# Performance work log

Measured on AMD Instinct MI355X. Metric: run time of the kernel, lower is better.

## Reference

```python
import jax, jax.numpy as jnp
import numpy as np

DIM = 1024
NUM_HEADS = 16
HEAD_DIM = DIM // NUM_HEADS
B, T = 2, 2048


def setup_inputs() -> dict:
    key = jax.random.key(0)
    ks = jax.random.split(key, 7)
    x = jax.random.normal(ks[0], (B, T, DIM), dtype=jnp.float32)
    # causal mask, broadcastable over batch and heads
    mask = jnp.tril(jnp.ones((T, T), dtype=bool))[None, None, :, :]
    # rope tables for half rotary angles, tiled to head_dim (cat of two halves)
    pos = jnp.arange(T, dtype=jnp.float32)[:, None]
    inv_freq = 1.0 / (10000.0 ** (jnp.arange(0, HEAD_DIM, 2, dtype=jnp.float32) / HEAD_DIM))
    ang = pos * inv_freq[None, :]                      # [T, hd/2]
    ang = jnp.concatenate([ang, ang], axis=-1)         # [T, hd]
    rope_sin = jnp.sin(ang)[None, None, :, :]
    rope_cos = jnp.cos(ang)[None, None, :, :]
    s = 0.02
    qkv_w = jax.random.normal(ks[1], (DIM, 3 * DIM), dtype=jnp.float32) * s
    qkv_b = jnp.zeros((3 * DIM,), dtype=jnp.float32)
    proj_w = jax.random.normal(ks[2], (DIM, DIM), dtype=jnp.float32) * s
    proj_b = jnp.zeros((DIM,), dtype=jnp.float32)
    return {"x": x, "mask": mask, "rope_sin": rope_sin, "rope_cos": rope_cos,
            "qkv_w": qkv_w, "qkv_b": qkv_b, "proj_w": proj_w, "proj_b": proj_b}


def _rotate_half(t):
    half = t.shape[-1] // 2
    return jnp.concatenate([-t[..., half:], t[..., :half]], axis=-1)


def _apply_rope(t, sin, cos):
    return t * cos + _rotate_half(t) * sin


def reference(x, mask, rope_sin, rope_cos, qkv_w, qkv_b, proj_w, proj_b):
    Bb, Tt, C = x.shape
    qkv = x @ qkv_w + qkv_b                            # [B, T, 3C]
    q, k, v = jnp.split(qkv, 3, axis=-1)
    def split_heads(t):                                # [B, T, C] -> [B, H, T, hd]
        return t.reshape(Bb, Tt, NUM_HEADS, HEAD_DIM).transpose(0, 2, 1, 3)
    q, k, v = split_heads(q), split_heads(k), split_heads(v)
    sin = rope_sin[:, :, :Tt, :]
    cos = rope_cos[:, :, :Tt, :]
    q = _apply_rope(q, sin, cos)
    k = _apply_rope(k, sin, cos)
    att = jnp.einsum("bhqd,bhkd->bhqk", q, k) / (HEAD_DIM ** 0.5)
    att = jnp.where(mask, att, -jnp.inf)
    att = jax.nn.softmax(att, axis=-1)
    y = jnp.einsum("bhqk,bhkd->bhqd", att, v)          # [B, H, T, hd]
    y = y.transpose(0, 2, 1, 3).reshape(Bb, Tt, C)
    return y @ proj_w + proj_b
```

## Files before the change

kernel.cpp:

```cpp
#include <hip/hip_runtime.h>

typedef unsigned short u16;
typedef u16 u16x8 __attribute__((ext_vector_type(8)));
typedef __bf16 bf16x8 __attribute__((ext_vector_type(8)));
typedef float f32x4 __attribute__((ext_vector_type(4)));

#define T_SEQ 2048
#define DIM 1024
#define NH 16
#define HD 64

#define MFMA(a, b, c) __builtin_amdgcn_mfma_f32_16x16x32_bf16(a, b, c, 0, 0, 0)

__device__ __forceinline__ u16 f2bf(float f) {
  return __builtin_bit_cast(u16, static_cast<__bf16>(f));
}

__device__ __forceinline__ bf16x8 ld8(const u16* p) {
  return __builtin_bit_cast(bf16x8, *(const u16x8*)p);
}

__device__ __forceinline__ void gload_lds16(const u16* g, u16* l) {
  __builtin_amdgcn_global_load_lds((const __attribute__((address_space(1))) void*)(g),
                                   (__attribute__((address_space(3))) void*)(l),
                                   16, 0, 0);
}

__global__ void k_prep(const float* __restrict__ X, u16* __restrict__ Y,
                       const float* __restrict__ Wq, u16* __restrict__ WqT,
                       const float* __restrict__ Wp, u16* __restrict__ WpT) {
  __shared__ float tile[32][33];
  int bid = blockIdx.x;
  if (bid < 4096) {
    int i = (bid * 256 + threadIdx.x) * 4;
    float4 f = *(const float4*)&X[i];
    ushort4 o = make_ushort4(f2bf(f.x), f2bf(f.y), f2bf(f.z), f2bf(f.w));
    *(ushort4*)&Y[i] = o;
    return;
  }
  const float* W; u16* WT; int K = 1024, N, bx, by;
  if (bid < 4096 + 3072) { int t = bid - 4096; W = Wq; WT = WqT; N = 3072; bx = t % 96; by = t / 96; }
  else                   { int t = bid - 7168; W = Wp; WT = WpT; N = 1024; bx = t % 32; by = t / 32; }
  int tx = threadIdx.x & 31, ty = threadIdx.x >> 5;
  int c0 = bx * 32, r0 = by * 32;
#pragma unroll
  for (int r = 0; r < 4; r++)
    tile[ty + r * 8][tx] = W[(r0 + ty + r * 8) * N + c0 + tx];
  __syncthreads();
#pragma unroll
  for (int r = 0; r < 4; r++)
    WT[(c0 + ty + r * 8) * K + r0 + tx] = f2bf(tile[tx][ty + r * 8]);
}


#define GEMM_STAGE3(buf, kk)                                                      \
  {                                                                               \
    _Pragma("unroll") for (int p = 0; p < 2; p++) {                               \
      int rr = w * 32 + p * 16;                                                   \
      gload_lds16(&Agp[(size_t)(rowBase + rr + srow) * Kd + (kk) + schunk],       \
                  &As[buf][rr * 32]);                                             \
      gload_lds16(&Bgp[(size_t)(colBase + rr + srow) * Kd + (kk) + schunk],       \
                  &Bs[buf][rr * 32]);                                             \
    }                                                                             \
  }

#define GEMM_COMPUTE3(buf)                                                        \
  {                                                                               \
    bf16x8 af[4], bfv[4];                                                         \
    _Pragma("unroll") for (int i = 0; i < 4; i++) {                               \
      af[i] = ld8(&As[buf][(wm * 64 + i * 16 + l15) * 32 + quad * 8]);            \
      bfv[i] = ld8(&Bs[buf][(wn * 64 + i * 16 + l15) * 32 + quad * 8]);           \
    }                                                                             \
    _Pragma("unroll") for (int i = 0; i < 4; i++)                                 \
        _Pragma("unroll") for (int j = 0; j < 4; j++)                             \
            acc[i][j] = MFMA(af[i], bfv[j], acc[i][j]);                           \
  }

#define GEMM_CORE3(Aptr, BTptr, bxv, byv)                                         \
  const int tid = threadIdx.x;                                                    \
  const int lane = tid & 63, w = tid >> 6;                                        \
  const int l15 = lane & 15, quad = lane >> 4;                                    \
  const int wm = w >> 1, wn = w & 1;                                              \
  const int rowBase = (byv) * 128;                                                \
  const int colBase = (bxv) * 128;                                                \
  const u16* Agp = (Aptr);                                                        \
  const u16* Bgp = (BTptr);                                                       \
  const int Kd = DIM;                                                             \
  f32x4 acc[4][4];                                                                \
  _Pragma("unroll") for (int i = 0; i < 4; i++)                                   \
      _Pragma("unroll") for (int j = 0; j < 4; j++)                               \
          acc[i][j] = (f32x4){0.f, 0.f, 0.f, 0.f};                                \
  const int srow = lane >> 2;                 \
  const int schunk = (lane & 3) * 8;    \
  GEMM_STAGE3(0, 0)                                                               \
  GEMM_STAGE3(1, 32)                                                              \
  _Pragma("unroll") for (int s = 0; s < 32; ++s) {                                \
    if (s < 31) { asm volatile("s_waitcnt vmcnt(4)" ::: "memory"); }              \
    else        { asm volatile("s_waitcnt vmcnt(0)" ::: "memory"); }              \
    __builtin_amdgcn_s_barrier();                                                 \
    if (s + 2 < 32) { GEMM_STAGE3((s + 2) % 3, (s + 2) * 32) }                    \
    GEMM_COMPUTE3(s % 3)                                                          \
  }                                                                               \
  __syncthreads();

#define EPLD 136

__global__ __launch_bounds__(256) void k_gemm_qkv(
    const u16* __restrict__ A, const u16* __restrict__ BT,
    const float* __restrict__ bias,
    const float* __restrict__ rsin, const float* __restrict__ rcos,
    u16* __restrict__ qb, u16* __restrict__ kb, u16* __restrict__ vtb) {
  __shared__ __align__(16) u16 LDSBUF[24576];
  u16 (*As)[128 * 32] = (u16(*)[128 * 32])(LDSBUF);
  u16 (*Bs)[128 * 32] = (u16(*)[128 * 32])(LDSBUF + 12288);
  const int n = blockIdx.x, xcd = n & 7, s = n >> 3;
  const int cg = xcd & 1, rg = xcd >> 1;
  const int bxv = cg * 12 + (s >> 3);
  const int byv = rg * 8 + (s & 7);
  GEMM_CORE3(A, BT, bxv, byv)

#pragma unroll
  for (int j = 0; j < 4; j++) {
    float bv = bias[colBase + wn * 64 + j * 16 + l15];
#pragma unroll
    for (int i = 0; i < 4; i++)
#pragma unroll
      for (int r = 0; r < 4; r++) acc[i][j][r] += bv;
  }

  const int colW = colBase + wn * 64;
  const int sec = colW >> 10;

  if (sec == 2) {
#pragma unroll
    for (int i = 0; i < 4; i++)
#pragma unroll
      for (int r = 0; r < 4; r++) {
        int tl = wm * 64 + i * 16 + quad * 4 + r;
#pragma unroll
        for (int j = 0; j < 4; j++) {
          int d2 = wn * 64 + j * 16 + l15;
          LDSBUF[d2 * EPLD + tl] = f2bf(acc[i][j][r]);
        }
      }
  } else {
#pragma unroll
    for (int i = 0; i < 4; i++)
#pragma unroll
      for (int r = 0; r < 4; r++) {
        int tl = wm * 64 + i * 16 + quad * 4 + r;
        int t = (rowBase + tl) & 2047;
#pragma unroll
        for (int j = 0; j < 4; j++) {
          int d = j * 16 + l15;
          float v = acc[i][j][r];
          float pr = acc[i][j ^ 2][r];
          float rot = (j < 2) ? -pr : pr;
          float rv = v * rcos[t * HD + d] + rot * rsin[t * HD + d];
          if (sec == 0) rv *= 0.18033688011112042f;
          LDSBUF[tl * EPLD + wn * 64 + d] = f2bf(rv);
        }
      }
  }
  __syncthreads();

  const int hb = (colBase & 1023) >> 6;
  const int b = rowBase >> 11, t0 = rowBase & 2047;
  if (sec == 2) {
#pragma unroll
    for (int p = 0; p < 8; p++) {
      int drow = (tid >> 4) + p * 16;
      int tc = (tid & 15) * 8;
      int hh = hb + (drow >> 6), d = drow & 63;
      u16x8 v = *(const u16x8*)&LDSBUF[drow * EPLD + tc];
      *(u16x8*)&vtb[((size_t)(b * NH + hh) * HD + d) * T_SEQ + t0 + tc] = v;
    }
  } else {
    u16* dst = (sec == 0) ? qb : kb;
#pragma unroll
    for (int p = 0; p < 8; p++) {
      int row = (tid >> 4) + p * 16;
      int dc = (tid & 15) * 8;
      int hh = hb + (dc >> 6), d = dc & 63;
      u16x8 v = *(const u16x8*)&LDSBUF[row * EPLD + dc];
      *(u16x8*)&dst[((size_t)(b * NH + hh) * T_SEQ + t0 + row) * HD + d] = v;
    }
  }
}

__global__ __launch_bounds__(256) void k_gemm_proj(
    const u16* __restrict__ A, const u16* __restrict__ BT,
    const float* __restrict__ bias, float* __restrict__ C) {
  __shared__ __align__(16) u16 AsP[3][4096];
  __shared__ __align__(16) u16 BsP[3][2048];
  const int n = blockIdx.x, xcd = n & 7, s = n >> 3;
  const int cg = xcd & 1, rg = xcd >> 1;
  const int bxv = cg * 8 + (s >> 3);
  const int byv = rg * 8 + (s & 7);
  const int tid = threadIdx.x;
  const int lane = tid & 63, w = tid >> 6;
  const int l15 = lane & 15, quad = lane >> 4;
  const int wm = w >> 1, wn = w & 1;
  const int rowBase = byv * 128;
  const int colBase = bxv * 64;
  const int srow = lane >> 2, schunk = (lane & 3) * 8;
  f32x4 acc[4][2];
#pragma unroll
  for (int i = 0; i < 4; i++)
#pragma unroll
    for (int j = 0; j < 2; j++) acc[i][j] = (f32x4){0.f, 0.f, 0.f, 0.f};

#define PROJ_STAGE(buf, kk)                                                       \
  {                                                                               \
    _Pragma("unroll") for (int p = 0; p < 2; p++) {                               \
      int rr = w * 32 + p * 16;                                                   \
      gload_lds16(&A[(size_t)(rowBase + rr + srow) * DIM + (kk) + schunk],        \
                  &AsP[buf][rr * 32]);                                            \
    }                                                                             \
    gload_lds16(&BT[(size_t)(colBase + w * 16 + srow) * DIM + (kk) + schunk],     \
                &BsP[buf][w * 16 * 32]);                                          \
  }
#define PROJ_COMPUTE(buf)                                                         \
  {                                                                               \
    bf16x8 af[4], bfv[2];                                                         \
    _Pragma("unroll") for (int i = 0; i < 4; i++)                                 \
        af[i] = ld8(&AsP[buf][(wm * 64 + i * 16 + l15) * 32 + quad * 8]);         \
    _Pragma("unroll") for (int j = 0; j < 2; j++)                                 \
        bfv[j] = ld8(&BsP[buf][(wn * 32 + j * 16 + l15) * 32 + quad * 8]);        \
    _Pragma("unroll") for (int i = 0; i < 4; i++)                                 \
        _Pragma("unroll") for (int j = 0; j < 2; j++)                             \
            acc[i][j] = MFMA(af[i], bfv[j], acc[i][j]);                           \
  }

  PROJ_STAGE(0, 0)
  PROJ_STAGE(1, 32)
#pragma unroll
  for (int s2 = 0; s2 < 32; ++s2) {
    if (s2 < 31) { asm volatile("s_waitcnt vmcnt(3)" ::: "memory"); }
    else         { asm volatile("s_waitcnt vmcnt(0)" ::: "memory"); }
    __builtin_amdgcn_s_barrier();
    if (s2 + 2 < 32) { PROJ_STAGE((s2 + 2) % 3, (s2 + 2) * 32) }
    PROJ_COMPUTE(s2 % 3)
  }

#pragma unroll
  for (int i = 0; i < 4; i++)
#pragma unroll
    for (int r = 0; r < 4; r++) {
      int grow = rowBase + wm * 64 + i * 16 + quad * 4 + r;
#pragma unroll
      for (int j = 0; j < 2; j++) {
        int col = colBase + wn * 32 + j * 16 + l15;
        C[grow * DIM + col] = acc[i][j][r] + bias[col];
      }
    }
}

#define KLD 72
#define VLD 136

__global__ __launch_bounds__(256, 3) void k_attn(
    const u16* __restrict__ qb, const u16* __restrict__ kb,
    const u16* __restrict__ vtb, u16* __restrict__ yb) {
  __shared__ __align__(16) u16 Ks[128 * KLD];
  __shared__ __align__(16) u16 VTs[64 * VLD];
  __shared__ __align__(16) u16 Ps[64 * VLD];
  const int tid = threadIdx.x;
  const int lane = tid & 63, w = tid >> 6;
  const int l15 = lane & 15, quad = lane >> 4;
  const int bh = blockIdx.x;
  const int qt = 31 - blockIdx.y;

  const u16* qp = qb + (size_t)bh * T_SEQ * HD;
  const u16* kp = kb + (size_t)bh * T_SEQ * HD;
  const u16* vp = vtb + (size_t)bh * HD * T_SEQ;

  const int nch = (qt + 2) >> 1;
  const int qrow_base = qt * 64 + w * 16 + quad * 4;

  const int sr = tid >> 3, sc = (tid & 7) * 8;
  const int vr = tid >> 4, vc = (tid & 15) * 8;

  u16x8 kreg[4], vreg[4];
#define LOADKV(c)                                                              \
  {                                                                            \
    _Pragma("unroll") for (int p = 0; p < 4; p++)                              \
        kreg[p] = *(const u16x8*)&kp[((c) * 128 + sr + p * 32) * HD + sc];     \
    _Pragma("unroll") for (int p = 0; p < 4; p++)                              \
        vreg[p] = *(const u16x8*)&vp[(vr + p * 16) * T_SEQ + (c) * 128 + vc];  \
  }
#define WRITEK()                                                               \
  {                                                                            \
    _Pragma("unroll") for (int p = 0; p < 4; p++)                              \
        *(u16x8*)&Ks[(sr + p * 32) * KLD + sc] = kreg[p];                      \
  }
#define WRITEV()                                                               \
  {                                                                            \
    _Pragma("unroll") for (int p = 0; p < 4; p++)                              \
        *(u16x8*)&VTs[(vr + p * 16) * VLD + vc] = vreg[p];                     \
  }

  LOADKV(0)

  {
#pragma unroll
    for (int p = 0; p < 2; p++) {
      int r = sr + p * 32;
      *(u16x8*)&Ps[r * KLD + sc] = *(const u16x8*)&qp[(qt * 64 + r) * HD + sc];
    }
  }
  __syncthreads();
  bf16x8 qa0 = ld8(&Ps[(w * 16 + l15) * KLD + quad * 8]);
  bf16x8 qa1 = ld8(&Ps[(w * 16 + l15) * KLD + 32 + quad * 8]);
  WRITEK()
  WRITEV()
  __syncthreads();

  f32x4 o[4];
#pragma unroll
  for (int j = 0; j < 4; j++) o[j] = (f32x4){0.f, 0.f, 0.f, 0.f};
  float li[4] = {0.f, 0.f, 0.f, 0.f};

  u16* ps = &Ps[w * 16 * VLD];
  const int srd = ((l15 & 1) << 3) | ((l15 >> 2) << 1) | ((l15 >> 1) & 1);

  for (int c = 0; c < nch; c++) {
    const bool more = (c + 1 < nch);
    if (more) LOADKV(c + 1)

    f32x4 s[8];
#pragma unroll
    for (int j = 0; j < 8; j++) {
      s[j] = (f32x4){0.f, 0.f, 0.f, 0.f};
      bf16x8 b0 = ld8(&Ks[(j * 16 + l15) * KLD + quad * 8]);
      bf16x8 b1 = ld8(&Ks[(j * 16 + l15) * KLD + 32 + quad * 8]);
      s[j] = MFMA(qa0, b0, s[j]);
      s[j] = MFMA(qa1, b1, s[j]);
    }

    if (more) {
      asm volatile("s_waitcnt lgkmcnt(0)" ::: "memory");
      __builtin_amdgcn_s_barrier();
      __builtin_amdgcn_sched_barrier(0);
      WRITEK()
    }

    const bool lastc = (c == nch - 1);
#pragma unroll
    for (int r = 0; r < 4; r++) {
      const int swr = ((r & 1) << 3) | (quad << 1) | (r >> 1);
#pragma unroll
      for (int j = 0; j < 8; j++) {
        float e;
        asm("v_exp_f32 %0, %1" : "=v"(e) : "v"(s[j][r]));
        if (lastc && (c * 128 + j * 16 + l15 > qrow_base + r)) e = 0.f;
        li[r] += e;
        ps[swr * VLD + j * 16 + l15] = f2bf(e);
      }
    }

#pragma unroll
    for (int c4 = 0; c4 < 4; c4++) {
      bf16x8 pa = ld8(&ps[srd * VLD + c4 * 32 + quad * 8]);
#pragma unroll
      for (int j2 = 0; j2 < 4; j2++) {
        bf16x8 vb = ld8(&VTs[(j2 * 16 + l15) * VLD + c4 * 32 + quad * 8]);
        o[j2] = MFMA(pa, vb, o[j2]);
      }
    }

    if (more) {
      __syncthreads();
      WRITEV()
    }
  }

#pragma unroll
  for (int r = 0; r < 4; r++) {
#pragma unroll
    for (int off = 8; off >= 1; off >>= 1) li[r] += __shfl_xor(li[r], off, 16);
    li[r] = 1.0f / li[r];
  }

#pragma unroll
  for (int j = 0; j < 4; j++)
#pragma unroll
    for (int r = 0; r < 4; r++) {
      const int swr = ((r & 1) << 3) | (quad << 1) | (r >> 1);
      ps[swr * VLD + j * 16 + l15] = f2bf(o[j][r] * li[r]);
    }
  __syncthreads();

  const int b = bh >> 4, h = bh & 15;
  {
    int sr2 = tid >> 3, sc2 = (tid & 7) * 8;
#pragma unroll
    for (int p = 0; p < 2; p++) {
      int row = sr2 + p * 32;
      int m = row & 15;
      int srow2 = ((m & 1) << 3) | ((m >> 2) << 1) | ((m >> 1) & 1);
      int t = qt * 64 + row;
      *(u16x8*)&yb[((size_t)(b * T_SEQ + t) * NH + h) * HD + sc2] =
          *(const u16x8*)&Ps[((row & 48) | srow2) * VLD + sc2];
    }
  }
}

extern "C" void kernel_launch(void* const* d_in, const int* in_sizes, int n_in,
                              void* d_out, int out_size, void* d_ws, size_t ws_size,
                              hipStream_t stream) {
  const float* x      = (const float*)d_in[0];
  const float* rsin   = (const float*)d_in[2];
  const float* rcos   = (const float*)d_in[3];
  const float* qkv_w  = (const float*)d_in[4];
  const float* qkv_b  = (const float*)d_in[5];
  const float* proj_w = (const float*)d_in[6];
  const float* proj_b = (const float*)d_in[7];
  float* out = (float*)d_out;

  char* ws = (char*)d_ws;
  u16* x_bf  = (u16*)(ws);
  u16* qkvT  = (u16*)(ws + (8ull << 20));
  u16* projT = (u16*)(ws + (14ull << 20));
  u16* q_buf = (u16*)(ws + (16ull << 20));
  u16* k_buf = (u16*)(ws + (24ull << 20));
  u16* vT    = (u16*)(ws + (32ull << 20));
  u16* y_buf = (u16*)(ws + (40ull << 20));

  hipLaunchKernelGGL(k_prep, dim3(8192), dim3(256), 0, stream,
                     x, x_bf, qkv_w, qkvT, proj_w, projT);
  hipLaunchKernelGGL(k_gemm_qkv, dim3(768), dim3(256), 0, stream,
                     x_bf, qkvT, qkv_b, rsin, rcos, q_buf, k_buf, vT);
  hipLaunchKernelGGL(k_attn, dim3(32, 32), dim3(256), 0, stream,
                     q_buf, k_buf, vT, y_buf);
  hipLaunchKernelGGL(k_gemm_proj, dim3(512), dim3(256), 0, stream,
                     y_buf, projT, proj_b, out);
}
```

Measured before the change: 188.3 us.

## Enlarge projection GEMM tile to 128x128, add MFMA priority hints in attention

The output projection GEMM moves from 256-thread blocks with 128x64 tiles to 512-thread blocks with 128x128 tiles. Each block stages A and B with one 16-byte load per thread per stage, and the grid shrinks to 256 blocks. This raises data reuse per block but leaves fewer blocks to spread across CUs. In attention, the MFMA sections are wrapped in s_setprio hints so waves doing matrix work get issue priority. The raw exp2 inline asm becomes __expf, with the Q prescale changed from 0.125·log2(e) to 0.125 so the math stays the same but each exponent costs an extra multiply.

```diff
diff --git a/kernel.cpp b/kernel.cpp
--- a/kernel.cpp
+++ b/kernel.cpp
@@ -157,7 +157,7 @@
           float pr = acc[i][j ^ 2][r];
           float rot = (j < 2) ? -pr : pr;
           float rv = v * rcos[t * HD + d] + rot * rsin[t * HD + d];
-          if (sec == 0) rv *= 0.18033688011112042f;
+          if (sec == 0) rv *= 0.125f;
           LDSBUF[tl * EPLD + wn * 64 + d] = f2bf(rv);
         }
       }
@@ -188,39 +188,36 @@
   }
 }
 
-__global__ __launch_bounds__(256) void k_gemm_proj(
+__global__ __launch_bounds__(512) void k_gemm_proj(
     const u16* __restrict__ A, const u16* __restrict__ BT,
     const float* __restrict__ bias, float* __restrict__ C) {
   __shared__ __align__(16) u16 AsP[3][4096];
-  __shared__ __align__(16) u16 BsP[3][2048];
+  __shared__ __align__(16) u16 BsP[3][4096];
   const int n = blockIdx.x, xcd = n & 7, s = n >> 3;
   const int cg = xcd & 1, rg = xcd >> 1;
-  const int bxv = cg * 8 + (s >> 3);
+  const int bxv = cg * 4 + (s >> 3);
   const int byv = rg * 8 + (s & 7);
   const int tid = threadIdx.x;
   const int lane = tid & 63, w = tid >> 6;
   const int l15 = lane & 15, quad = lane >> 4;
-  const int wm = w >> 1, wn = w & 1;
-  const int rowBase = byv * 128;
-  const int colBase = bxv * 64;
-  const int srow = lane >> 2, schunk = (lane & 3) * 8;
+  const int wm = w >> 2, wn = w & 3;
+  const int rowBase = byv * 128, colBase = bxv * 128;
+  const int strow = tid >> 2;
+  const int stchunk = (tid & 3) * 8;
   f32x4 acc[4][2];
 #pragma unroll
   for (int i = 0; i < 4; i++)
 #pragma unroll
     for (int j = 0; j < 2; j++) acc[i][j] = (f32x4){0.f, 0.f, 0.f, 0.f};
 
-#define PROJ_STAGE(buf, kk)                                                       \
+#define PROJ_STAGE8(buf, kk)                                                      \
   {                                                                               \
-    _Pragma("unroll") for (int p = 0; p < 2; p++) {                               \
-      int rr = w * 32 + p * 16;                                                   \
-      gload_lds16(&A[(size_t)(rowBase + rr + srow) * DIM + (kk) + schunk],        \
-                  &AsP[buf][rr * 32]);                                            \
-    }                                                                             \
-    gload_lds16(&BT[(size_t)(colBase + w * 16 + srow) * DIM + (kk) + schunk],     \
-                &BsP[buf][w * 16 * 32]);                                          \
-  }
-#define PROJ_COMPUTE(buf)                                                         \
+    gload_lds16(&A[(size_t)(rowBase + strow) * DIM + (kk) + stchunk],             \
+                &AsP[buf][w * 512]);                                              \
+    gload_lds16(&BT[(size_t)(colBase + strow) * DIM + (kk) + stchunk],            \
+                &BsP[buf][w * 512]);                                              \
+  }
+#define PROJ_COMPUTE8(buf)                                                        \
   {                                                                               \
     bf16x8 af[4], bfv[2];                                                         \
     _Pragma("unroll") for (int i = 0; i < 4; i++)                                 \
@@ -232,15 +229,15 @@
             acc[i][j] = MFMA(af[i], bfv[j], acc[i][j]);                           \
   }
 
-  PROJ_STAGE(0, 0)
-  PROJ_STAGE(1, 32)
+  PROJ_STAGE8(0, 0)
+  PROJ_STAGE8(1, 32)
 #pragma unroll
   for (int s2 = 0; s2 < 32; ++s2) {
-    if (s2 < 31) { asm volatile("s_waitcnt vmcnt(3)" ::: "memory"); }
+    if (s2 < 31) { asm volatile("s_waitcnt vmcnt(2)" ::: "memory"); }
     else         { asm volatile("s_waitcnt vmcnt(0)" ::: "memory"); }
     __builtin_amdgcn_s_barrier();
-    if (s2 + 2 < 32) { PROJ_STAGE((s2 + 2) % 3, (s2 + 2) * 32) }
-    PROJ_COMPUTE(s2 % 3)
+    if (s2 + 2 < 32) { PROJ_STAGE8((s2 + 2) % 3, (s2 + 2) * 32) }
+    PROJ_COMPUTE8(s2 % 3)
   }
 
 #pragma unroll
@@ -329,6 +326,7 @@
     if (more) LOADKV(c + 1)
 
     f32x4 s[8];
+    __builtin_amdgcn_s_setprio(1);
 #pragma unroll
     for (int j = 0; j < 8; j++) {
       s[j] = (f32x4){0.f, 0.f, 0.f, 0.f};
@@ -337,6 +335,7 @@
       s[j] = MFMA(qa0, b0, s[j]);
       s[j] = MFMA(qa1, b1, s[j]);
     }
+    __builtin_amdgcn_s_setprio(0);
 
     if (more) {
       asm volatile("s_waitcnt lgkmcnt(0)" ::: "memory");
@@ -351,14 +350,14 @@
       const int swr = ((r & 1) << 3) | (quad << 1) | (r >> 1);
 #pragma unroll
       for (int j = 0; j < 8; j++) {
-        float e;
-        asm("v_exp_f32 %0, %1" : "=v"(e) : "v"(s[j][r]));
+        float e = __expf(s[j][r]);
         if (lastc && (c * 128 + j * 16 + l15 > qrow_base + r)) e = 0.f;
         li[r] += e;
         ps[swr * VLD + j * 16 + l15] = f2bf(e);
       }
     }
 
+    __builtin_amdgcn_s_setprio(1);
 #pragma unroll
     for (int c4 = 0; c4 < 4; c4++) {
       bf16x8 pa = ld8(&ps[srd * VLD + c4 * 32 + quad * 8]);
@@ -368,6 +367,7 @@
         o[j2] = MFMA(pa, vb, o[j2]);
       }
     }
+    __builtin_amdgcn_s_setprio(0);
 
     if (more) {
       __syncthreads();
@@ -433,6 +433,6 @@
                      x_bf, qkvT, qkv_b, rsin, rcos, q_buf, k_buf, vT);
   hipLaunchKernelGGL(k_attn, dim3(32, 32), dim3(256), 0, stream,
                      q_buf, k_buf, vT, y_buf);
-  hipLaunchKernelGGL(k_gemm_proj, dim3(512), dim3(256), 0, stream,
+  hipLaunchKernelGGL(k_gemm_proj, dim3(256), dim3(512), 0, stream,
                      y_buf, projT, proj_b, out);
 }
```

After: 186.6 us. About the same (-0.9%).
